# Kernel tuning notes

Measured on AMD Instinct MI355X. Metric: run time of the kernel, lower is better.

Reference implementation:

```python
import jax, jax.numpy as jnp
import numpy as np

jax.config.update("jax_enable_x64", True)

SR = 24000
NCH = 64
F_MIN, F_MAX = 10.0, 100.0
R_MIN, R_MAX = 0.9999, 0.99999
ALIGN_W, RAW_W = 10.0, 0.1
FFT_CFG = [(512, 128), (1024, 256), (2048, 512)]  # (n_fft==win_length, hop)
EPS = 1e-7

# deterministic IIR coefficients (buffers in the torch module)
_freqs = np.exp(np.linspace(np.log(F_MIN), np.log(F_MAX), NCH))
_radii = np.linspace(R_MIN, R_MAX, NCH)
_theta = 2.0 * np.pi * _freqs / SR
A1 = jnp.asarray(-2.0 * _radii * np.cos(_theta), jnp.float64)  # [C]
A2 = jnp.asarray(_radii ** 2, jnp.float64)                      # [C]
B0 = jnp.asarray((1.0 - _radii) * 0.5, jnp.float64)             # [C]


def _iir(x):
    # x: [B,1,T] float32 -> causal 2nd-order IIR per channel in float64 -> [B,C,T] float32
    B, _, T = x.shape
    xd = jnp.broadcast_to(x.astype(jnp.float64), (B, NCH, T))
    xt = jnp.moveaxis(xd, 2, 0)  # [T,B,C]
    z = jnp.zeros((B, NCH), jnp.float64)

    def step(carry, xn):
        y1, y2 = carry
        y = B0 * xn - A1 * y1 - A2 * y2  # y[n] = b0*x[n] - a1*y[n-1] - a2*y[n-2]
        return (y, y1), y

    _, ys = jax.lax.scan(step, (z, z), xt)
    return jnp.moveaxis(ys, 0, 2).astype(jnp.float32)  # [B,C,T]


def _probe(x):
    fwd = _iir(x)
    bwd = jnp.flip(_iir(jnp.flip(x, axis=-1)), axis=-1)
    return jnp.concatenate([fwd, bwd], axis=1)  # [B,2C,T]


def _stft_mag(x1d, n_fft, hop):
    # torch.stft(center=False, window=None) == rectangular frames + rfft
    T = x1d.shape[-1]
    n_frames = 1 + (T - n_fft) // hop
    idx = np.arange(n_frames)[:, None] * hop + np.arange(n_fft)[None, :]
    frames = x1d[:, idx]  # [B, n_frames, n_fft]
    return jnp.abs(jnp.fft.rfft(frames, axis=-1)) + EPS


def _mss_loss(pred, target):
    loss = jnp.float32(0.0)
    xp, xt = pred[:, 0, :], target[:, 0, :]
    for n_fft, hop in FFT_CFG:
        xm = _stft_mag(xp, n_fft, hop)
        ym = _stft_mag(xt, n_fft, hop)
        loss = loss + jnp.mean(jnp.abs(xm - ym)) + jnp.mean(jnp.abs(jnp.log(xm) - jnp.log(ym)))
    return loss


def setup_inputs() -> dict:
    key = jax.random.key(0)
    k1, k2, k3 = jax.random.split(key, 3)
    pred = jax.random.normal(k1, (4, 1, 48000), dtype=jnp.float32)
    target = jax.random.normal(k2, (4, 1, 48000), dtype=jnp.float32)
    # orthogonal init of the frozen Tank mixing matrix [out=64, in=128]
    g = jax.random.normal(k3, (128, 64), dtype=jnp.float32)
    q, _ = jnp.linalg.qr(g)
    W = q.T.astype(jnp.float32)  # [64,128], rows orthonormal
    return {"pred": pred, "target": target, "W": W}


def reference(pred, target, W):
    T = pred.shape[-1]
    m = T // 3
    l_mss = _mss_loss(pred, target)

    tank = lambda h: jnp.tanh(jnp.einsum('bct,oc->bot', h, W))  # Linear on [B,T,2C] then tanh
    p_emb = tank(_probe(pred))
    t_emb = tank(_probe(target))
    l_align = jnp.mean(jnp.abs(p_emb[..., m:-m] - t_emb[..., m:-m]))
    l_raw = jnp.mean(jnp.abs(pred[..., m:-m] - target[..., m:-m])) * RAW_W
    total = l_mss + l_align * ALIGN_W + l_raw
    return (total, l_mss, l_align)
```

## Files before the change

### kernel.cpp

```cpp
#include <hip/hip_runtime.h>

#define T_LEN 48000
#define NSEQ  1024
#define LC    100
#define NCHK  320
#define GRP   16
#define NGRP  20

#define NB_F2048 360
#define NB_F1024 736
#define NB_F512  744
#define NB_FFT   1840
#define NB_P1    1280
#define NB_EMB   250
#define NFRAMES  2584

using short8 = __attribute__((ext_vector_type(8))) short;
using f32x4  = __attribute__((ext_vector_type(4))) float;

__device__ __forceinline__ void chan_params(int ch, double& a1, double& a2, double& b0) {
    const double lf = log(10.0) + (double)ch * (log(100.0) - log(10.0)) / 63.0;
    const double f  = exp(lf);
    const double r  = 0.9999 + (double)ch * (0.99999 - 0.9999) / 63.0;
    const double th = 2.0 * 3.14159265358979323846 * f / 24000.0;
    a1 = -2.0 * r * cos(th);
    a2 = r * r;
    b0 = (1.0 - r) * 0.5;
}

__device__ __forceinline__ unsigned short f32_to_bf16(float f) {
    unsigned u = __float_as_uint(f);
    u += 0x7fffu + ((u >> 16) & 1u);
    return (unsigned short)(u >> 16);
}

__device__ __forceinline__ float fast_tanh(float x) {
    const float e = __expf(2.0f * x);
    return 1.0f - 2.0f / (e + 1.0f);
}

__device__ __forceinline__ float2 cmul(float2 a, float2 b) {
    return make_float2(a.x * b.x - a.y * b.y, a.x * b.y + a.y * b.x);
}
__device__ __forceinline__ float2 cadd(float2 a, float2 b) { return make_float2(a.x + b.x, a.y + b.y); }
__device__ __forceinline__ float2 csub(float2 a, float2 b) { return make_float2(a.x - b.x, a.y - b.y); }

__global__ void setup_kernel(double* __restrict__ cst) {
    const int t = threadIdx.x;
    if (t < 64) {
        double a1, a2, b0; chan_params(t, a1, a2, b0);
        double m00 = -a1, m01 = -a2, m10 = 1.0, m11 = 0.0;
        double r00 = 1.0, r01 = 0.0, r10 = 0.0, r11 = 1.0;
        int e = LC;
        while (e) {
            if (e & 1) {
                const double t00 = r00 * m00 + r01 * m10, t01 = r00 * m01 + r01 * m11;
                const double t10 = r10 * m00 + r11 * m10, t11 = r10 * m01 + r11 * m11;
                r00 = t00; r01 = t01; r10 = t10; r11 = t11;
            }
            const double q00 = m00 * m00 + m01 * m10, q01 = m00 * m01 + m01 * m11;
            const double q10 = m10 * m00 + m11 * m10, q11 = m10 * m01 + m11 * m11;
            m00 = q00; m01 = q01; m10 = q10; m11 = q11;
            e >>= 1;
        }
        cst[t * 16 + 0] = a1; cst[t * 16 + 1] = a2; cst[t * 16 + 2] = b0;
        cst[t * 16 + 3] = r00; cst[t * 16 + 4] = r01;
        cst[t * 16 + 5] = r10; cst[t * 16 + 6] = r11;
        double q00 = r00, q01 = r01, q10 = r10, q11 = r11;
        #pragma unroll
        for (int s = 0; s < 4; ++s) {
            const double n00 = q00 * q00 + q01 * q10, n01 = q00 * q01 + q01 * q11;
            const double n10 = q10 * q00 + q11 * q10, n11 = q10 * q01 + q11 * q11;
            q00 = n00; q01 = n01; q10 = n10; q11 = n11;
        }
        cst[t * 16 + 7] = q00; cst[t * 16 + 8]  = q01;
        cst[t * 16 + 9] = q10; cst[t * 16 + 10] = q11;
    }
}

__global__ __launch_bounds__(256) void phase1_kernel(const float* __restrict__ pred,
                                                     const float* __restrict__ target,
                                                     const double* __restrict__ cst,
                                                     float2* __restrict__ P,
                                                     double* __restrict__ fftP) {
    __shared__ float2 bufA[2048];
    __shared__ float2 bufB[2048];
    __shared__ float2 twl[512];
    __shared__ float redw[4];
    const int blk = blockIdx.x;

    if (blk < NB_FFT) {
        int N, HOP, frame0, nthr, lt, off;
        double scale;
        const int tid = threadIdx.x;
        if (blk < NB_F2048) {
            N = 2048; HOP = 512; scale = 1.0 / (4.0 * 90.0 * 1025.0);
            frame0 = blk; nthr = 256; lt = tid; off = 0;
        } else if (blk < NB_F2048 + NB_F1024) {
            N = 1024; HOP = 256; scale = 1.0 / (4.0 * 184.0 * 513.0);
            frame0 = blk; nthr = 256; lt = tid; off = 0;
        } else {
            N = 512;  HOP = 128; scale = 1.0 / (4.0 * 372.0 * 257.0);
            const int id = blk - (NB_F2048 + NB_F1024);
            frame0 = NB_F2048 + NB_F1024 + 2 * id + (tid >> 7);
            nthr = 128; lt = tid & 127; off = (tid >> 7) << 9;
        }
        int fidL;
        if (blk < NB_F2048) fidL = frame0;
        else if (blk < NB_F2048 + NB_F1024) fidL = frame0 - NB_F2048;
        else fidL = frame0 - (NB_F2048 + NB_F1024);
        const int b  = fidL & 3;
        const int fr = fidL >> 2;
        const int N4 = N >> 2;
        const float* xp = pred   + b * T_LEN + fr * HOP;
        const float* xt = target + b * T_LEN + fr * HOP;

        const float wstep = -6.283185307179586f / (float)N;
        for (int k = tid; k < N4; k += 256) {
            float sn, cs; __sincosf(wstep * (float)k, &sn, &cs);
            twl[k] = make_float2(cs, sn);
        }
        for (int i = lt; i < N; i += nthr) bufA[off + i] = make_float2(xp[i], xt[i]);
        __syncthreads();

        float2* X = bufA; float2* Y = bufB;
        int s = 1, ls = 0;
        while ((s << 2) <= N) {
            for (int i = lt; i < N4; i += nthr) {
                const int p  = i >> ls;
                const int q  = i & (s - 1);
                const int k1 = p << ls;
                const float2 a0 = X[off + i];
                const float2 a1 = X[off + i + N4];
                const float2 a2 = X[off + i + 2 * N4];
                const float2 a3 = X[off + i + 3 * N4];
                const float2 w1 = twl[k1];
                const int   k2 = k1 << 1;
                const float2 t2 = twl[k2 & (N4 - 1)];
                const float2 w2 = (k2 < N4) ? t2 : make_float2(t2.y, -t2.x);
                const float2 e1 = cadd(a0, a2), d1 = csub(a0, a2);
                const float2 e2 = cadd(a1, a3), d2 = csub(a1, a3);
                const float2 o1 = cmul(d1, w1);
                const float2 ot = cmul(d2, w1);
                const float2 o2 = make_float2(ot.y, -ot.x);
                const float2 E1 = cadd(e1, e2);
                const float2 O1 = cmul(csub(e1, e2), w2);
                const float2 E2 = cadd(o1, o2);
                const float2 O2 = cmul(csub(o1, o2), w2);
                const int o4 = q + (p << (ls + 2));
                Y[off + o4]         = E1;
                Y[off + o4 + s]     = E2;
                Y[off + o4 + 2 * s] = O1;
                Y[off + o4 + 3 * s] = O2;
            }
            __syncthreads();
            float2* t = X; X = Y; Y = t;
            s <<= 2; ls += 2;
        }
        const bool rad2 = (s < N);
        const int  half = N >> 1;

        float ss = 0.f;
        for (int k = lt; k <= half; k += nthr) {
            const int k2 = (N - k) & (N - 1);
            float2 zk, zn;
            if (rad2) {
                zk = (k  < half) ? cadd(X[off + k],  X[off + k  + half]) : csub(X[off + k  - half], X[off + k]);
                zn = (k2 < half) ? cadd(X[off + k2], X[off + k2 + half]) : csub(X[off + k2 - half], X[off + k2]);
            } else {
                zk = X[off + k]; zn = X[off + k2];
            }
            const float xpr = 0.5f * (zk.x + zn.x), xpi = 0.5f * (zk.y - zn.y);
            const float xtr = 0.5f * (zk.y + zn.y), xti = 0.5f * (zn.x - zk.x);
            const float xm = sqrtf(xpr * xpr + xpi * xpi) + 1e-7f;
            const float ym = sqrtf(xtr * xtr + xti * xti) + 1e-7f;
            ss += fabsf(xm - ym) + fabsf(__logf(xm) - __logf(ym));
        }
        for (int o = 32; o >= 1; o >>= 1) ss += __shfl_down(ss, o, 64);
        const int lane = tid & 63, wv = tid >> 6;
        if (lane == 0) redw[wv] = ss;
        __syncthreads();
        if (nthr == 256) {
            if (tid == 0)
                fftP[frame0] = ((double)redw[0] + (double)redw[1] +
                                (double)redw[2] + (double)redw[3]) * scale;
        } else {
            if (lt == 0)
                fftP[frame0] = ((double)redw[(tid >> 7) * 2] +
                                (double)redw[(tid >> 7) * 2 + 1]) * scale;
        }
        return;
    }

    const int tid   = (blk - NB_FFT) * 256 + threadIdx.x;
    const int seq   = tid & (NSEQ - 1);
    const int chunk = tid >> 10;
    const int ch  = seq & 63;
    const int dir = (seq >> 6) & 1;
    const int b   = (seq >> 7) & 3;
    const int sg  = seq >> 9;
    const float a1f = (float)cst[ch * 16 + 0];
    const float a2f = (float)cst[ch * 16 + 1];
    const float b0f = (float)cst[ch * 16 + 2];
    const float* x = (sg ? target : pred) + b * T_LEN;
    const int n0   = chunk * LC;
    const int base = dir ? (T_LEN - 1 - n0) : n0;
    const int stp  = dir ? -1 : 1;
    float y1 = 0.f, y2 = 0.f;
    #pragma unroll 4
    for (int i = 0; i < LC; ++i) {
        const float xv = x[base + stp * i];
        const float y  = b0f * xv - a1f * y1 - a2f * y2;
        y2 = y1; y1 = y;
    }
    P[chunk * NSEQ + seq] = make_float2(y1, y2);
}

__global__ __launch_bounds__(256) void iir_scanA(const double* __restrict__ cst,
                                                 const float2* __restrict__ P,
                                                 float2* __restrict__ Tg) {
    const int tid = blockIdx.x * 256 + threadIdx.x;
    const int seq = tid & (NSEQ - 1);
    const int g   = tid >> 10;
    const int ch  = seq & 63;
    const double A00 = cst[ch * 16 + 3], A01 = cst[ch * 16 + 4];
    const double A10 = cst[ch * 16 + 5], A11 = cst[ch * 16 + 6];
    double t1 = 0.0, t2 = 0.0;
    #pragma unroll
    for (int j = 0; j < GRP; ++j) {
        const float2 p = P[(g * GRP + j) * NSEQ + seq];
        const double n1 = A00 * t1 + A01 * t2 + (double)p.x;
        const double n2 = A10 * t1 + A11 * t2 + (double)p.y;
        t1 = n1; t2 = n2;
    }
    Tg[g * NSEQ + seq] = make_float2((float)t1, (float)t2);
}

__global__ __launch_bounds__(256) void iir_pass2(const float* __restrict__ pred,
                                                 const float* __restrict__ target,
                                                 const double* __restrict__ cst,
                                                 const float2* __restrict__ P,
                                                 const float2* __restrict__ Tg,
                                                 unsigned short* __restrict__ H) {
    const int tid = blockIdx.x * 256 + threadIdx.x;
    const int seq = tid & (NSEQ - 1);
    const int c   = 160 + (tid >> 10);
    const int ch  = seq & 63;
    const int dir = (seq >> 6) & 1;
    const int b   = (seq >> 7) & 3;
    const int sg  = seq >> 9;
    const double A00 = cst[ch * 16 + 3], A01 = cst[ch * 16 + 4];
    const double A10 = cst[ch * 16 + 5], A11 = cst[ch * 16 + 6];
    const double B00 = cst[ch * 16 + 7], B01 = cst[ch * 16 + 8];
    const double B10 = cst[ch * 16 + 9], B11 = cst[ch * 16 + 10];

    const int g = c >> 4;
    double y1 = 0.0, y2 = 0.0;
    for (int j = 0; j < g; ++j) {
        const float2 t = Tg[j * NSEQ + seq];
        const double n1 = B00 * y1 + B01 * y2 + (double)t.x;
        const double n2 = B10 * y1 + B11 * y2 + (double)t.y;
        y1 = n1; y2 = n2;
    }
    for (int k = g * GRP; k < c; ++k) {
        const float2 p = P[k * NSEQ + seq];
        const double n1 = A00 * y1 + A01 * y2 + (double)p.x;
        const double n2 = A10 * y1 + A11 * y2 + (double)p.y;
        y1 = n1; y2 = n2;
    }

    const float a1f = (float)cst[ch * 16 + 0];
    const float a2f = (float)cst[ch * 16 + 1];
    const float b0f = (float)cst[ch * 16 + 2];
    float y1f = (float)y1, y2f = (float)y2;
    const float* x = (sg ? target : pred) + b * T_LEN;
    const int n0 = c * LC;
    unsigned short* Hb = H + (size_t)(sg * 4 + b) * 16000 * 128 + (dir * 64 + ch);
    if (dir == 0) {
        #pragma unroll 4
        for (int i = 0; i < LC; ++i) {
            const int n = n0 + i;
            const float xv = x[n];
            const float y  = b0f * xv - a1f * y1f - a2f * y2f;
            Hb[(size_t)(n - 16000) * 128] = f32_to_bf16(y);
            y2f = y1f; y1f = y;
        }
    } else {
        #pragma unroll 4
        for (int i = 0; i < LC; ++i) {
            const int n = n0 + i;
            const float xv = x[T_LEN - 1 - n];
            const float y  = b0f * xv - a1f * y1f - a2f * y2f;
            Hb[(size_t)(31999 - n) * 128] = f32_to_bf16(y);
            y2f = y1f; y1f = y;
        }
    }
}

__global__ __launch_bounds__(256) void embed_kernel(const float* __restrict__ W,
                                                    const unsigned short* __restrict__ H,
                                                    const float* __restrict__ pred,
                                                    const float* __restrict__ target,
                                                    double2* __restrict__ emP) {
    __shared__ double em[8];
    float rsum;
    {
        const int i  = blockIdx.x * 256 + threadIdx.x;
        const int bb = i / 16000;
        const int t  = i - bb * 16000 + 16000;
        rsum = fabsf(pred[bb * T_LEN + t] - target[bb * T_LEN + t]);
        for (int off = 32; off >= 1; off >>= 1) rsum += __shfl_down(rsum, off, 64);
    }

    const int lane = threadIdx.x & 63;
    const int wave = threadIdx.x >> 6;
    const int gw   = blockIdx.x * 4 + wave;
    const int row  = lane & 15;
    const int quad = lane >> 4;

    short8 A[4][4];
    #pragma unroll
    for (int mi = 0; mi < 4; ++mi)
        #pragma unroll
        for (int ki = 0; ki < 4; ++ki) {
            const float* wp = W + (mi * 16 + row) * 128 + ki * 32 + quad * 8;
            short8 a;
            #pragma unroll
            for (int j = 0; j < 8; ++j) a[j] = (short)f32_to_bf16(wp[j]);
            A[mi][ki] = a;
        }

    float lsum = 0.f;
    const int t0 = gw * 16;
    for (int b = 0; b < 4; ++b) {
        const unsigned short* hp = H + (size_t)(b * 16000 + t0 + row) * 128 + quad * 8;
        const unsigned short* ht = hp + (size_t)4 * 16000 * 128;
        f32x4 accp[4], acct[4];
        #pragma unroll
        for (int mi = 0; mi < 4; ++mi) {
            accp[mi] = f32x4{0.f, 0.f, 0.f, 0.f};
            acct[mi] = f32x4{0.f, 0.f, 0.f, 0.f};
        }
        #pragma unroll
        for (int ki = 0; ki < 4; ++ki) {
            const short8 bp = *(const short8*)(hp + ki * 32);
            const short8 bt = *(const short8*)(ht + ki * 32);
            #pragma unroll
            for (int mi = 0; mi < 4; ++mi) {
                accp[mi] = __builtin_amdgcn_mfma_f32_16x16x32_bf16(A[mi][ki], bp, accp[mi], 0, 0, 0);
                acct[mi] = __builtin_amdgcn_mfma_f32_16x16x32_bf16(A[mi][ki], bt, acct[mi], 0, 0, 0);
            }
        }
        #pragma unroll
        for (int mi = 0; mi < 4; ++mi)
            #pragma unroll
            for (int r = 0; r < 4; ++r) {
                const float ep = fast_tanh(accp[mi][r]);
                const float et = fast_tanh(acct[mi][r]);
                lsum += fabsf(ep - et);
            }
    }
    for (int off = 32; off >= 1; off >>= 1) lsum += __shfl_down(lsum, off, 64);
    if (lane == 0) { em[wave] = (double)lsum; em[wave + 4] = (double)rsum; }
    __syncthreads();
    if (threadIdx.x == 0)
        emP[blockIdx.x] = make_double2(em[0] + em[1] + em[2] + em[3],
                                       em[4] + em[5] + em[6] + em[7]);
}

__global__ __launch_bounds__(256) void finalize_kernel(const double* __restrict__ fftP,
                                                       const double2* __restrict__ emP,
                                                       float* __restrict__ out) {
    __shared__ double red[256];
    const int tid = threadIdx.x;
    double lm = 0.0;
    for (int i = tid; i < NFRAMES; i += 256) lm += fftP[i];
    double la = 0.0, lr = 0.0;
    for (int i = tid; i < NB_EMB; i += 256) { const double2 e = emP[i]; la += e.x; lr += e.y; }

    red[tid] = lm; __syncthreads();
    for (int o = 128; o > 0; o >>= 1) { if (tid < o) red[tid] += red[tid + o]; __syncthreads(); }
    lm = red[0]; __syncthreads();
    red[tid] = la; __syncthreads();
    for (int o = 128; o > 0; o >>= 1) { if (tid < o) red[tid] += red[tid + o]; __syncthreads(); }
    la = red[0]; __syncthreads();
    red[tid] = lr; __syncthreads();
    for (int o = 128; o > 0; o >>= 1) { if (tid < o) red[tid] += red[tid + o]; __syncthreads(); }
    if (tid == 0) {
        lr = red[0] / 64000.0 * 0.1;
        la = la / (4.0 * 64.0 * 16000.0);
        out[0] = (float)(lm + 10.0 * la + lr);
        out[1] = (float)lm;
        out[2] = (float)la;
    }
}

extern "C" void kernel_launch(void* const* d_in, const int* in_sizes, int n_in,
                              void* d_out, int out_size, void* d_ws, size_t ws_size,
                              hipStream_t stream) {
    const float* pred   = (const float*)d_in[0];
    const float* target = (const float*)d_in[1];
    const float* W      = (const float*)d_in[2];
    float* out = (float*)d_out;

    char* ws = (char*)d_ws;
    double*  cst  = (double*)ws;
    double*  fftP = (double*)(ws + 8192);
    double2* emP  = (double2*)(ws + 28928);
    float2*  P    = (float2*)(ws + 33280);
    float2*  Tg   = (float2*)(ws + 2654720);
    unsigned short* H = (unsigned short*)(ws + 2818560);

    hipLaunchKernelGGL(setup_kernel,  dim3(1), dim3(64), 0, stream, cst);
    hipLaunchKernelGGL(phase1_kernel, dim3(NB_FFT + NB_P1), dim3(256), 0, stream, pred, target, cst, P, fftP);
    hipLaunchKernelGGL(iir_scanA,     dim3(NGRP * 4), dim3(256), 0, stream, cst, P, Tg);
    hipLaunchKernelGGL(iir_pass2,     dim3(640), dim3(256), 0, stream, pred, target, cst, P, Tg, H);
    hipLaunchKernelGGL(embed_kernel,  dim3(NB_EMB), dim3(256), 0, stream, W, H, pred, target, emP);
    hipLaunchKernelGGL(finalize_kernel, dim3(1), dim3(256), 0, stream, fftP, emP, out);
}
```

Measured before the change: 126.4 us.

## Merge kernels with atomic-counter handoffs and recompute IIR constants inline

Removes the setup kernel by having each thread compute channel coefficients and matrix powers itself, using a Taylor cosine. Fuses the scan and pass2 kernels into one launch, where the pass2 blocks spin on an atomic counter until the scan blocks finish. Folds finalize into the embed kernel with a last-block-done pattern. This cuts the launch count from six to three, at the cost of redundant double-precision math per thread and a spin-wait that depends on the scan blocks being scheduled first.

```diff
diff --git a/kernel.cpp b/kernel.cpp
--- a/kernel.cpp
+++ b/kernel.cpp
@@ -9,23 +9,56 @@
 
 #define NB_F2048 360
 #define NB_F1024 736
-#define NB_F512  744
 #define NB_FFT   1840
 #define NB_P1    1280
+#define NB_SCANA 80
+#define NB_PASS2 640
 #define NB_EMB   250
 #define NFRAMES  2584
 
 using short8 = __attribute__((ext_vector_type(8))) short;
 using f32x4  = __attribute__((ext_vector_type(4))) float;
+
+__device__ __forceinline__ double cos_small(double t) {
+    const double t2 = t * t;
+    return 1.0 - t2 * (0.5 - t2 * ((1.0 / 24.0) - t2 * (1.0 / 720.0)));
+}
 
 __device__ __forceinline__ void chan_params(int ch, double& a1, double& a2, double& b0) {
     const double lf = log(10.0) + (double)ch * (log(100.0) - log(10.0)) / 63.0;
     const double f  = exp(lf);
     const double r  = 0.9999 + (double)ch * (0.99999 - 0.9999) / 63.0;
     const double th = 2.0 * 3.14159265358979323846 * f / 24000.0;
-    a1 = -2.0 * r * cos(th);
+    a1 = -2.0 * r * cos_small(th);
     a2 = r * r;
     b0 = (1.0 - r) * 0.5;
+}
+
+__device__ __forceinline__ void mat_powLC(double a1, double a2,
+                                          double& r00, double& r01, double& r10, double& r11) {
+    double m00 = -a1, m01 = -a2, m10 = 1.0, m11 = 0.0;
+    r00 = 1.0; r01 = 0.0; r10 = 0.0; r11 = 1.0;
+    int e = LC;
+    while (e) {
+        if (e & 1) {
+            const double t00 = r00 * m00 + r01 * m10, t01 = r00 * m01 + r01 * m11;
+            const double t10 = r10 * m00 + r11 * m10, t11 = r10 * m01 + r11 * m11;
+            r00 = t00; r01 = t01; r10 = t10; r11 = t11;
+        }
+        const double q00 = m00 * m00 + m01 * m10, q01 = m00 * m01 + m01 * m11;
+        const double q10 = m10 * m00 + m11 * m10, q11 = m10 * m01 + m11 * m11;
+        m00 = q00; m01 = q01; m10 = q10; m11 = q11;
+        e >>= 1;
+    }
+}
+
+__device__ __forceinline__ void mat_sq4(double& q00, double& q01, double& q10, double& q11) {
+    #pragma unroll
+    for (int s = 0; s < 4; ++s) {
+        const double n00 = q00 * q00 + q01 * q10, n01 = q00 * q01 + q01 * q11;
+        const double n10 = q10 * q00 + q11 * q10, n11 = q10 * q01 + q11 * q11;
+        q00 = n00; q01 = n01; q10 = n10; q11 = n11;
+    }
 }
 
 __device__ __forceinline__ unsigned short f32_to_bf16(float f) {
@@ -45,49 +78,18 @@
 __device__ __forceinline__ float2 cadd(float2 a, float2 b) { return make_float2(a.x + b.x, a.y + b.y); }
 __device__ __forceinline__ float2 csub(float2 a, float2 b) { return make_float2(a.x - b.x, a.y - b.y); }
 
-__global__ void setup_kernel(double* __restrict__ cst) {
-    const int t = threadIdx.x;
-    if (t < 64) {
-        double a1, a2, b0; chan_params(t, a1, a2, b0);
-        double m00 = -a1, m01 = -a2, m10 = 1.0, m11 = 0.0;
-        double r00 = 1.0, r01 = 0.0, r10 = 0.0, r11 = 1.0;
-        int e = LC;
-        while (e) {
-            if (e & 1) {
-                const double t00 = r00 * m00 + r01 * m10, t01 = r00 * m01 + r01 * m11;
-                const double t10 = r10 * m00 + r11 * m10, t11 = r10 * m01 + r11 * m11;
-                r00 = t00; r01 = t01; r10 = t10; r11 = t11;
-            }
-            const double q00 = m00 * m00 + m01 * m10, q01 = m00 * m01 + m01 * m11;
-            const double q10 = m10 * m00 + m11 * m10, q11 = m10 * m01 + m11 * m11;
-            m00 = q00; m01 = q01; m10 = q10; m11 = q11;
-            e >>= 1;
-        }
-        cst[t * 16 + 0] = a1; cst[t * 16 + 1] = a2; cst[t * 16 + 2] = b0;
-        cst[t * 16 + 3] = r00; cst[t * 16 + 4] = r01;
-        cst[t * 16 + 5] = r10; cst[t * 16 + 6] = r11;
-        double q00 = r00, q01 = r01, q10 = r10, q11 = r11;
-        #pragma unroll
-        for (int s = 0; s < 4; ++s) {
-            const double n00 = q00 * q00 + q01 * q10, n01 = q00 * q01 + q01 * q11;
-            const double n10 = q10 * q00 + q11 * q10, n11 = q10 * q01 + q11 * q11;
-            q00 = n00; q01 = n01; q10 = n10; q11 = n11;
-        }
-        cst[t * 16 + 7] = q00; cst[t * 16 + 8]  = q01;
-        cst[t * 16 + 9] = q10; cst[t * 16 + 10] = q11;
-    }
-}
-
 __global__ __launch_bounds__(256) void phase1_kernel(const float* __restrict__ pred,
                                                      const float* __restrict__ target,
-                                                     const double* __restrict__ cst,
                                                      float2* __restrict__ P,
-                                                     double* __restrict__ fftP) {
+                                                     double* __restrict__ fftP,
+                                                     int* __restrict__ ctr) {
     __shared__ float2 bufA[2048];
     __shared__ float2 bufB[2048];
     __shared__ float2 twl[512];
     __shared__ float redw[4];
     const int blk = blockIdx.x;
+
+    if (blk == 0 && threadIdx.x == 0) { ctr[0] = 0; ctr[1] = 0; }
 
     if (blk < NB_FFT) {
         int N, HOP, frame0, nthr, lt, off;
@@ -199,9 +201,8 @@
     const int dir = (seq >> 6) & 1;
     const int b   = (seq >> 7) & 3;
     const int sg  = seq >> 9;
-    const float a1f = (float)cst[ch * 16 + 0];
-    const float a2f = (float)cst[ch * 16 + 1];
-    const float b0f = (float)cst[ch * 16 + 2];
+    double a1, a2, b0; chan_params(ch, a1, a2, b0);
+    const float a1f = (float)a1, a2f = (float)a2, b0f = (float)b0;
     const float* x = (sg ? target : pred) + b * T_LEN;
     const int n0   = chunk * LC;
     const int base = dir ? (T_LEN - 1 - n0) : n0;
@@ -216,43 +217,56 @@
     P[chunk * NSEQ + seq] = make_float2(y1, y2);
 }
 
-__global__ __launch_bounds__(256) void iir_scanA(const double* __restrict__ cst,
-                                                 const float2* __restrict__ P,
-                                                 float2* __restrict__ Tg) {
-    const int tid = blockIdx.x * 256 + threadIdx.x;
-    const int seq = tid & (NSEQ - 1);
-    const int g   = tid >> 10;
-    const int ch  = seq & 63;
-    const double A00 = cst[ch * 16 + 3], A01 = cst[ch * 16 + 4];
-    const double A10 = cst[ch * 16 + 5], A11 = cst[ch * 16 + 6];
-    double t1 = 0.0, t2 = 0.0;
-    #pragma unroll
-    for (int j = 0; j < GRP; ++j) {
-        const float2 p = P[(g * GRP + j) * NSEQ + seq];
-        const double n1 = A00 * t1 + A01 * t2 + (double)p.x;
-        const double n2 = A10 * t1 + A11 * t2 + (double)p.y;
-        t1 = n1; t2 = n2;
-    }
-    Tg[g * NSEQ + seq] = make_float2((float)t1, (float)t2);
-}
-
-__global__ __launch_bounds__(256) void iir_pass2(const float* __restrict__ pred,
-                                                 const float* __restrict__ target,
-                                                 const double* __restrict__ cst,
-                                                 const float2* __restrict__ P,
-                                                 const float2* __restrict__ Tg,
-                                                 unsigned short* __restrict__ H) {
-    const int tid = blockIdx.x * 256 + threadIdx.x;
+__global__ __launch_bounds__(256, 4) void scan2_kernel(const float* __restrict__ pred,
+                                                       const float* __restrict__ target,
+                                                       const float2* __restrict__ P,
+                                                       float2* __restrict__ Tg,
+                                                       unsigned short* __restrict__ H,
+                                                       int* __restrict__ ctr) {
+    const int blk = blockIdx.x;
+    if (blk < NB_SCANA) {
+        const int tid = blk * 256 + threadIdx.x;
+        const int seq = tid & (NSEQ - 1);
+        const int g   = tid >> 10;
+        const int ch  = seq & 63;
+        double a1, a2, b0; chan_params(ch, a1, a2, b0);
+        double A00, A01, A10, A11; mat_powLC(a1, a2, A00, A01, A10, A11);
+        double t1 = 0.0, t2 = 0.0;
+        #pragma unroll
+        for (int j = 0; j < GRP; ++j) {
+            const float2 p = P[(g * GRP + j) * NSEQ + seq];
+            const double n1 = A00 * t1 + A01 * t2 + (double)p.x;
+            const double n2 = A10 * t1 + A11 * t2 + (double)p.y;
+            t1 = n1; t2 = n2;
+        }
+        Tg[g * NSEQ + seq] = make_float2((float)t1, (float)t2);
+        __syncthreads();
+        __threadfence();
+        if (threadIdx.x == 0)
+            __hip_atomic_fetch_add(&ctr[0], 1, __ATOMIC_RELEASE, __HIP_MEMORY_SCOPE_AGENT);
+        return;
+    }
+
+    const int tid = (blk - NB_SCANA) * 256 + threadIdx.x;
     const int seq = tid & (NSEQ - 1);
     const int c   = 160 + (tid >> 10);
     const int ch  = seq & 63;
     const int dir = (seq >> 6) & 1;
     const int b   = (seq >> 7) & 3;
     const int sg  = seq >> 9;
-    const double A00 = cst[ch * 16 + 3], A01 = cst[ch * 16 + 4];
-    const double A10 = cst[ch * 16 + 5], A11 = cst[ch * 16 + 6];
-    const double B00 = cst[ch * 16 + 7], B01 = cst[ch * 16 + 8];
-    const double B10 = cst[ch * 16 + 9], B11 = cst[ch * 16 + 10];
+    double a1, a2, b0; chan_params(ch, a1, a2, b0);
+    double A00, A01, A10, A11; mat_powLC(a1, a2, A00, A01, A10, A11);
+    double B00 = A00, B01 = A01, B10 = A10, B11 = A11; mat_sq4(B00, B01, B10, B11);
+    const float a1f = (float)a1, a2f = (float)a2, b0f = (float)b0;
+
+    if (threadIdx.x == 0) {
+        long spins = 0;
+        while (__hip_atomic_load(&ctr[0], __ATOMIC_ACQUIRE, __HIP_MEMORY_SCOPE_AGENT) < NB_SCANA) {
+            __builtin_amdgcn_s_sleep(8);
+            if (++spins > (1L << 26)) break;
+        }
+    }
+    __syncthreads();
 
     const int g = c >> 4;
     double y1 = 0.0, y2 = 0.0;
@@ -269,9 +283,6 @@
         y1 = n1; y2 = n2;
     }
 
-    const float a1f = (float)cst[ch * 16 + 0];
-    const float a2f = (float)cst[ch * 16 + 1];
-    const float b0f = (float)cst[ch * 16 + 2];
     float y1f = (float)y1, y2f = (float)y2;
     const float* x = (sg ? target : pred) + b * T_LEN;
     const int n0 = c * LC;
@@ -301,8 +312,13 @@
                                                     const unsigned short* __restrict__ H,
                                                     const float* __restrict__ pred,
                                                     const float* __restrict__ target,
-                                                    double2* __restrict__ emP) {
+                                                    double2* __restrict__ emP,
+                                                    const double* __restrict__ fftP,
+                                                    float* __restrict__ out,
+                                                    int* __restrict__ ctr) {
     __shared__ double em[8];
+    __shared__ double red[256];
+    __shared__ int lastFlag;
     float rsum;
     {
         const int i  = blockIdx.x * 256 + threadIdx.x;
@@ -363,35 +379,35 @@
     for (int off = 32; off >= 1; off >>= 1) lsum += __shfl_down(lsum, off, 64);
     if (lane == 0) { em[wave] = (double)lsum; em[wave + 4] = (double)rsum; }
     __syncthreads();
-    if (threadIdx.x == 0)
+    if (threadIdx.x == 0) {
         emP[blockIdx.x] = make_double2(em[0] + em[1] + em[2] + em[3],
                                        em[4] + em[5] + em[6] + em[7]);
-}
-
-__global__ __launch_bounds__(256) void finalize_kernel(const double* __restrict__ fftP,
-                                                       const double2* __restrict__ emP,
-                                                       float* __restrict__ out) {
-    __shared__ double red[256];
-    const int tid = threadIdx.x;
-    double lm = 0.0;
-    for (int i = tid; i < NFRAMES; i += 256) lm += fftP[i];
-    double la = 0.0, lr = 0.0;
-    for (int i = tid; i < NB_EMB; i += 256) { const double2 e = emP[i]; la += e.x; lr += e.y; }
-
-    red[tid] = lm; __syncthreads();
-    for (int o = 128; o > 0; o >>= 1) { if (tid < o) red[tid] += red[tid + o]; __syncthreads(); }
-    lm = red[0]; __syncthreads();
-    red[tid] = la; __syncthreads();
-    for (int o = 128; o > 0; o >>= 1) { if (tid < o) red[tid] += red[tid + o]; __syncthreads(); }
-    la = red[0]; __syncthreads();
-    red[tid] = lr; __syncthreads();
-    for (int o = 128; o > 0; o >>= 1) { if (tid < o) red[tid] += red[tid + o]; __syncthreads(); }
-    if (tid == 0) {
-        lr = red[0] / 64000.0 * 0.1;
-        la = la / (4.0 * 64.0 * 16000.0);
-        out[0] = (float)(lm + 10.0 * la + lr);
-        out[1] = (float)lm;
-        out[2] = (float)la;
+        __threadfence();
+        const int done = __hip_atomic_fetch_add(&ctr[1], 1, __ATOMIC_ACQ_REL, __HIP_MEMORY_SCOPE_AGENT);
+        lastFlag = (done == NB_EMB - 1);
+    }
+    __syncthreads();
+
+    if (lastFlag) {
+        const int tid = threadIdx.x;
+        double lm = 0.0, la = 0.0, lr = 0.0;
+        for (int i = tid; i < NFRAMES; i += 256) lm += fftP[i];
+        for (int i = tid; i < NB_EMB; i += 256) { const double2 e = emP[i]; la += e.x; lr += e.y; }
+        red[tid] = lm; __syncthreads();
+        for (int o = 128; o > 0; o >>= 1) { if (tid < o) red[tid] += red[tid + o]; __syncthreads(); }
+        lm = red[0]; __syncthreads();
+        red[tid] = la; __syncthreads();
+        for (int o = 128; o > 0; o >>= 1) { if (tid < o) red[tid] += red[tid + o]; __syncthreads(); }
+        la = red[0]; __syncthreads();
+        red[tid] = lr; __syncthreads();
+        for (int o = 128; o > 0; o >>= 1) { if (tid < o) red[tid] += red[tid + o]; __syncthreads(); }
+        if (tid == 0) {
+            lr = red[0] / 64000.0 * 0.1;
+            la = la / (4.0 * 64.0 * 16000.0);
+            out[0] = (float)(lm + 10.0 * la + lr);
+            out[1] = (float)lm;
+            out[2] = (float)la;
+        }
     }
 }
 
@@ -404,17 +420,17 @@
     float* out = (float*)d_out;
 
     char* ws = (char*)d_ws;
-    double*  cst  = (double*)ws;
-    double*  fftP = (double*)(ws + 8192);
-    double2* emP  = (double2*)(ws + 28928);
-    float2*  P    = (float2*)(ws + 33280);
-    float2*  Tg   = (float2*)(ws + 2654720);
-    unsigned short* H = (unsigned short*)(ws + 2818560);
-
-    hipLaunchKernelGGL(setup_kernel,  dim3(1), dim3(64), 0, stream, cst);
-    hipLaunchKernelGGL(phase1_kernel, dim3(NB_FFT + NB_P1), dim3(256), 0, stream, pred, target, cst, P, fftP);
-    hipLaunchKernelGGL(iir_scanA,     dim3(NGRP * 4), dim3(256), 0, stream, cst, P, Tg);
-    hipLaunchKernelGGL(iir_pass2,     dim3(640), dim3(256), 0, stream, pred, target, cst, P, Tg, H);
-    hipLaunchKernelGGL(embed_kernel,  dim3(NB_EMB), dim3(256), 0, stream, W, H, pred, target, emP);
-    hipLaunchKernelGGL(finalize_kernel, dim3(1), dim3(256), 0, stream, fftP, emP, out);
-}
+    int*     ctr  = (int*)ws;
+    double*  fftP = (double*)(ws + 256);
+    double2* emP  = (double2*)(ws + 21504);
+    float2*  P    = (float2*)(ws + 25600);
+    float2*  Tg   = (float2*)(ws + 2647040);
+    unsigned short* H = (unsigned short*)(ws + 2810880);
+
+    hipLaunchKernelGGL(phase1_kernel, dim3(NB_FFT + NB_P1), dim3(256), 0, stream,
+                       pred, target, P, fftP, ctr);
+    hipLaunchKernelGGL(scan2_kernel, dim3(NB_SCANA + NB_PASS2), dim3(256), 0, stream,
+                       pred, target, P, Tg, H, ctr);
+    hipLaunchKernelGGL(embed_kernel, dim3(NB_EMB), dim3(256), 0, stream,
+                       W, H, pred, target, emP, fftP, out, ctr);
+}
```

After: 166.4 us. 31.7% more time.

## Fuse IIR pass2, embedding GEMM and finalize into one kernel via LDS tiles

Applied to the files above, without the earlier changes.

Merges the second IIR pass with the tanh-embedding MFMA step. Each block now computes a 100-sample time tile for all 128 probe columns of both signals, stores it in shared memory as bf16, and runs the GEMM directly from LDS, so the large H intermediate no longer makes a round trip through global memory. The finalize reduction moves into the last block, which is picked with an atomic counter, removing two kernel launches. The cost is padding work (7 16-row tiles for 100 rows, with zeroed pad rows), smaller GEMM tiles with W reloaded in every block, and LDS pressure that may limit occupancy.

```diff
diff --git a/kernel.cpp b/kernel.cpp
--- a/kernel.cpp
+++ b/kernel.cpp
@@ -9,10 +9,10 @@
 
 #define NB_F2048 360
 #define NB_F1024 736
-#define NB_F512  744
 #define NB_FFT   1840
 #define NB_P1    1280
-#define NB_EMB   250
+#define NB_SCANA 80
+#define NB_FUSED 640
 #define NFRAMES  2584
 
 using short8 = __attribute__((ext_vector_type(8))) short;
@@ -45,8 +45,9 @@
 __device__ __forceinline__ float2 cadd(float2 a, float2 b) { return make_float2(a.x + b.x, a.y + b.y); }
 __device__ __forceinline__ float2 csub(float2 a, float2 b) { return make_float2(a.x - b.x, a.y - b.y); }
 
-__global__ void setup_kernel(double* __restrict__ cst) {
+__global__ void setup_kernel(double* __restrict__ cst, int* __restrict__ ctr) {
     const int t = threadIdx.x;
+    if (t == 0) { ctr[0] = 0; }
     if (t < 64) {
         double a1, a2, b0; chan_params(t, a1, a2, b0);
         double m00 = -a1, m01 = -a2, m10 = 1.0, m11 = 0.0;
@@ -216,9 +217,9 @@
     P[chunk * NSEQ + seq] = make_float2(y1, y2);
 }
 
-__global__ __launch_bounds__(256) void iir_scanA(const double* __restrict__ cst,
-                                                 const float2* __restrict__ P,
-                                                 float2* __restrict__ Tg) {
+__global__ __launch_bounds__(256) void scanA_kernel(const double* __restrict__ cst,
+                                                    const float2* __restrict__ P,
+                                                    float2* __restrict__ Tg) {
     const int tid = blockIdx.x * 256 + threadIdx.x;
     const int seq = tid & (NSEQ - 1);
     const int g   = tid >> 10;
@@ -236,23 +237,43 @@
     Tg[g * NSEQ + seq] = make_float2((float)t1, (float)t2);
 }
 
-__global__ __launch_bounds__(256) void iir_pass2(const float* __restrict__ pred,
-                                                 const float* __restrict__ target,
-                                                 const double* __restrict__ cst,
-                                                 const float2* __restrict__ P,
-                                                 const float2* __restrict__ Tg,
-                                                 unsigned short* __restrict__ H) {
-    const int tid = blockIdx.x * 256 + threadIdx.x;
-    const int seq = tid & (NSEQ - 1);
-    const int c   = 160 + (tid >> 10);
-    const int ch  = seq & 63;
-    const int dir = (seq >> 6) & 1;
-    const int b   = (seq >> 7) & 3;
-    const int sg  = seq >> 9;
+__global__ __launch_bounds__(256) void p2embed_kernel(const float* __restrict__ pred,
+                                                      const float* __restrict__ target,
+                                                      const double* __restrict__ cst,
+                                                      const float2* __restrict__ P,
+                                                      const float2* __restrict__ Tg,
+                                                      const float* __restrict__ W,
+                                                      double2* __restrict__ emP,
+                                                      const double* __restrict__ fftP,
+                                                      float* __restrict__ out,
+                                                      int* __restrict__ ctr) {
+    __shared__ unsigned short Hs[2][112][136];
+    __shared__ double em[8];
+    __shared__ double red[256];
+    __shared__ int lastFlag;
+
+    const int blk = blockIdx.x;
+    const int b   = blk & 3;
+    const int ci  = blk >> 2;
+    const int tid = threadIdx.x;
+    const int ch  = tid & 63;
+    const int dir = (tid >> 6) & 1;
+    const int sg  = tid >> 7;
+    const int T0  = ci * 100;
+
+    const int c   = dir ? (319 - ci) : (ci + 160);
+    const int seq = sg * 512 + b * 128 + dir * 64 + ch;
+
     const double A00 = cst[ch * 16 + 3], A01 = cst[ch * 16 + 4];
     const double A10 = cst[ch * 16 + 5], A11 = cst[ch * 16 + 6];
     const double B00 = cst[ch * 16 + 7], B01 = cst[ch * 16 + 8];
     const double B10 = cst[ch * 16 + 9], B11 = cst[ch * 16 + 10];
+
+    for (int z = tid; z < 2 * 12 * 128; z += 256) {
+        const int zsg = z / (12 * 128);
+        const int rem = z % (12 * 128);
+        Hs[zsg][100 + rem / 128][rem % 128] = 0;
+    }
 
     const int g = c >> 4;
     double y1 = 0.0, y2 = 0.0;
@@ -275,123 +296,98 @@
     float y1f = (float)y1, y2f = (float)y2;
     const float* x = (sg ? target : pred) + b * T_LEN;
     const int n0 = c * LC;
-    unsigned short* Hb = H + (size_t)(sg * 4 + b) * 16000 * 128 + (dir * 64 + ch);
+    const int col = dir * 64 + ch;
     if (dir == 0) {
         #pragma unroll 4
         for (int i = 0; i < LC; ++i) {
-            const int n = n0 + i;
-            const float xv = x[n];
+            const float xv = x[n0 + i];
             const float y  = b0f * xv - a1f * y1f - a2f * y2f;
-            Hb[(size_t)(n - 16000) * 128] = f32_to_bf16(y);
+            Hs[sg][i][col] = f32_to_bf16(y);
             y2f = y1f; y1f = y;
         }
     } else {
         #pragma unroll 4
         for (int i = 0; i < LC; ++i) {
-            const int n = n0 + i;
-            const float xv = x[T_LEN - 1 - n];
+            const float xv = x[T_LEN - 1 - (n0 + i)];
             const float y  = b0f * xv - a1f * y1f - a2f * y2f;
-            Hb[(size_t)(31999 - n) * 128] = f32_to_bf16(y);
+            Hs[sg][99 - i][col] = f32_to_bf16(y);
             y2f = y1f; y1f = y;
         }
     }
-}
-
-__global__ __launch_bounds__(256) void embed_kernel(const float* __restrict__ W,
-                                                    const unsigned short* __restrict__ H,
-                                                    const float* __restrict__ pred,
-                                                    const float* __restrict__ target,
-                                                    double2* __restrict__ emP) {
-    __shared__ double em[8];
-    float rsum;
-    {
-        const int i  = blockIdx.x * 256 + threadIdx.x;
-        const int bb = i / 16000;
-        const int t  = i - bb * 16000 + 16000;
-        rsum = fabsf(pred[bb * T_LEN + t] - target[bb * T_LEN + t]);
-        for (int off = 32; off >= 1; off >>= 1) rsum += __shfl_down(rsum, off, 64);
-    }
-
-    const int lane = threadIdx.x & 63;
-    const int wave = threadIdx.x >> 6;
-    const int gw   = blockIdx.x * 4 + wave;
+
+    float rsum = 0.f;
+    if (tid < 100) {
+        const int n = 16000 + T0 + tid;
+        rsum = fabsf(pred[b * T_LEN + n] - target[b * T_LEN + n]);
+    }
+    __syncthreads();
+
+    const int lane = tid & 63;
+    const int wave = tid >> 6;
     const int row  = lane & 15;
     const int quad = lane >> 4;
 
-    short8 A[4][4];
+    short8 Af[4];
     #pragma unroll
-    for (int mi = 0; mi < 4; ++mi)
+    for (int ki = 0; ki < 4; ++ki) {
+        const float* wp = W + (wave * 16 + row) * 128 + ki * 32 + quad * 8;
+        short8 a;
+        #pragma unroll
+        for (int j = 0; j < 8; ++j) a[j] = (short)f32_to_bf16(wp[j]);
+        Af[ki] = a;
+    }
+
+    float lsum = 0.f;
+    #pragma unroll
+    for (int nt = 0; nt < 7; ++nt) {
+        f32x4 accp = f32x4{0.f, 0.f, 0.f, 0.f};
+        f32x4 acct = f32x4{0.f, 0.f, 0.f, 0.f};
         #pragma unroll
         for (int ki = 0; ki < 4; ++ki) {
-            const float* wp = W + (mi * 16 + row) * 128 + ki * 32 + quad * 8;
-            short8 a;
-            #pragma unroll
-            for (int j = 0; j < 8; ++j) a[j] = (short)f32_to_bf16(wp[j]);
-            A[mi][ki] = a;
-        }
-
-    float lsum = 0.f;
-    const int t0 = gw * 16;
-    for (int b = 0; b < 4; ++b) {
-        const unsigned short* hp = H + (size_t)(b * 16000 + t0 + row) * 128 + quad * 8;
-        const unsigned short* ht = hp + (size_t)4 * 16000 * 128;
-        f32x4 accp[4], acct[4];
+            const short8 bp = *(const short8*)&Hs[0][nt * 16 + row][ki * 32 + quad * 8];
+            const short8 bt = *(const short8*)&Hs[1][nt * 16 + row][ki * 32 + quad * 8];
+            accp = __builtin_amdgcn_mfma_f32_16x16x32_bf16(Af[ki], bp, accp, 0, 0, 0);
+            acct = __builtin_amdgcn_mfma_f32_16x16x32_bf16(Af[ki], bt, acct, 0, 0, 0);
+        }
         #pragma unroll
-        for (int mi = 0; mi < 4; ++mi) {
-            accp[mi] = f32x4{0.f, 0.f, 0.f, 0.f};
-            acct[mi] = f32x4{0.f, 0.f, 0.f, 0.f};
-        }
-        #pragma unroll
-        for (int ki = 0; ki < 4; ++ki) {
-            const short8 bp = *(const short8*)(hp + ki * 32);
-            const short8 bt = *(const short8*)(ht + ki * 32);
-            #pragma unroll
-            for (int mi = 0; mi < 4; ++mi) {
-                accp[mi] = __builtin_amdgcn_mfma_f32_16x16x32_bf16(A[mi][ki], bp, accp[mi], 0, 0, 0);
-                acct[mi] = __builtin_amdgcn_mfma_f32_16x16x32_bf16(A[mi][ki], bt, acct[mi], 0, 0, 0);
-            }
-        }
-        #pragma unroll
-        for (int mi = 0; mi < 4; ++mi)
-            #pragma unroll
-            for (int r = 0; r < 4; ++r) {
-                const float ep = fast_tanh(accp[mi][r]);
-                const float et = fast_tanh(acct[mi][r]);
-                lsum += fabsf(ep - et);
-            }
-    }
-    for (int off = 32; off >= 1; off >>= 1) lsum += __shfl_down(lsum, off, 64);
+        for (int r = 0; r < 4; ++r)
+            lsum += fabsf(fast_tanh(accp[r]) - fast_tanh(acct[r]));
+    }
+
+    for (int o = 32; o >= 1; o >>= 1) {
+        lsum += __shfl_down(lsum, o, 64);
+        rsum += __shfl_down(rsum, o, 64);
+    }
     if (lane == 0) { em[wave] = (double)lsum; em[wave + 4] = (double)rsum; }
     __syncthreads();
-    if (threadIdx.x == 0)
-        emP[blockIdx.x] = make_double2(em[0] + em[1] + em[2] + em[3],
-                                       em[4] + em[5] + em[6] + em[7]);
-}
-
-__global__ __launch_bounds__(256) void finalize_kernel(const double* __restrict__ fftP,
-                                                       const double2* __restrict__ emP,
-                                                       float* __restrict__ out) {
-    __shared__ double red[256];
-    const int tid = threadIdx.x;
-    double lm = 0.0;
-    for (int i = tid; i < NFRAMES; i += 256) lm += fftP[i];
-    double la = 0.0, lr = 0.0;
-    for (int i = tid; i < NB_EMB; i += 256) { const double2 e = emP[i]; la += e.x; lr += e.y; }
-
-    red[tid] = lm; __syncthreads();
-    for (int o = 128; o > 0; o >>= 1) { if (tid < o) red[tid] += red[tid + o]; __syncthreads(); }
-    lm = red[0]; __syncthreads();
-    red[tid] = la; __syncthreads();
-    for (int o = 128; o > 0; o >>= 1) { if (tid < o) red[tid] += red[tid + o]; __syncthreads(); }
-    la = red[0]; __syncthreads();
-    red[tid] = lr; __syncthreads();
-    for (int o = 128; o > 0; o >>= 1) { if (tid < o) red[tid] += red[tid + o]; __syncthreads(); }
     if (tid == 0) {
-        lr = red[0] / 64000.0 * 0.1;
-        la = la / (4.0 * 64.0 * 16000.0);
-        out[0] = (float)(lm + 10.0 * la + lr);
-        out[1] = (float)lm;
-        out[2] = (float)la;
+        emP[blk] = make_double2(em[0] + em[1] + em[2] + em[3],
+                                em[4] + em[5] + em[6] + em[7]);
+        __threadfence();
+        const int done = __hip_atomic_fetch_add(&ctr[0], 1, __ATOMIC_ACQ_REL, __HIP_MEMORY_SCOPE_AGENT);
+        lastFlag = (done == NB_FUSED - 1);
+    }
+    __syncthreads();
+
+    if (lastFlag) {
+        double lm = 0.0, la = 0.0, lr = 0.0;
+        for (int i = tid; i < NFRAMES; i += 256) lm += fftP[i];
+        for (int i = tid; i < NB_FUSED; i += 256) { const double2 e = emP[i]; la += e.x; lr += e.y; }
+        red[tid] = lm; __syncthreads();
+        for (int o = 128; o > 0; o >>= 1) { if (tid < o) red[tid] += red[tid + o]; __syncthreads(); }
+        lm = red[0]; __syncthreads();
+        red[tid] = la; __syncthreads();
+        for (int o = 128; o > 0; o >>= 1) { if (tid < o) red[tid] += red[tid + o]; __syncthreads(); }
+        la = red[0]; __syncthreads();
+        red[tid] = lr; __syncthreads();
+        for (int o = 128; o > 0; o >>= 1) { if (tid < o) red[tid] += red[tid + o]; __syncthreads(); }
+        if (tid == 0) {
+            lr = red[0] / 64000.0 * 0.1;
+            la = la / (4.0 * 64.0 * 16000.0);
+            out[0] = (float)(lm + 10.0 * la + lr);
+            out[1] = (float)lm;
+            out[2] = (float)la;
+        }
     }
 }
 
@@ -404,17 +400,17 @@
     float* out = (float*)d_out;
 
     char* ws = (char*)d_ws;
-    double*  cst  = (double*)ws;
-    double*  fftP = (double*)(ws + 8192);
-    double2* emP  = (double2*)(ws + 28928);
-    float2*  P    = (float2*)(ws + 33280);
-    float2*  Tg   = (float2*)(ws + 2654720);
-    unsigned short* H = (unsigned short*)(ws + 2818560);
-
-    hipLaunchKernelGGL(setup_kernel,  dim3(1), dim3(64), 0, stream, cst);
-    hipLaunchKernelGGL(phase1_kernel, dim3(NB_FFT + NB_P1), dim3(256), 0, stream, pred, target, cst, P, fftP);
-    hipLaunchKernelGGL(iir_scanA,     dim3(NGRP * 4), dim3(256), 0, stream, cst, P, Tg);
-    hipLaunchKernelGGL(iir_pass2,     dim3(640), dim3(256), 0, stream, pred, target, cst, P, Tg, H);
-    hipLaunchKernelGGL(embed_kernel,  dim3(NB_EMB), dim3(256), 0, stream, W, H, pred, target, emP);
-    hipLaunchKernelGGL(finalize_kernel, dim3(1), dim3(256), 0, stream, fftP, emP, out);
-}
+    int*     ctr  = (int*)ws;
+    double*  cst  = (double*)(ws + 256);
+    double*  fftP = (double*)(ws + 8448);
+    double2* emP  = (double2*)(ws + 29184);
+    float2*  P    = (float2*)(ws + 39936);
+    float2*  Tg   = (float2*)(ws + 2661376);
+
+    hipLaunchKernelGGL(setup_kernel,  dim3(1), dim3(64), 0, stream, cst, ctr);
+    hipLaunchKernelGGL(phase1_kernel, dim3(NB_FFT + NB_P1), dim3(256), 0, stream,
+                       pred, target, cst, P, fftP);
+    hipLaunchKernelGGL(scanA_kernel, dim3(NB_SCANA), dim3(256), 0, stream, cst, P, Tg);
+    hipLaunchKernelGGL(p2embed_kernel, dim3(NB_FUSED), dim3(256), 0, stream,
+                       pred, target, cst, P, Tg, W, emP, fftP, out, ctr);
+}
```

Measured after the change: 136.8 us. +8.3%, slower.
